# Kernel tuning notes

Measured on AMD Instinct MI355X. Metric: run time of the kernel, lower is better.

## Reference

```python
import jax, jax.numpy as jnp
import numpy as np

B, S, C, HD = 2, 4096, 2048, 128
H = C // HD  # 16 heads
EPS = 1.1920929e-07  # torch RMSNorm default eps for float32 (finfo.eps)


def _make_rope(seq_len, head_dim):
    # Standard RoPE 2x2 rotation matrices: [1, S, 1, head_dim//2, 2, 2]
    half = head_dim // 2
    freqs = 1.0 / (10000.0 ** (np.arange(0, half, dtype=np.float32) / half))
    ang = np.arange(seq_len, dtype=np.float32)[:, None] * freqs[None, :]  # [S, half]
    cos, sin = np.cos(ang), np.sin(ang)
    rot = np.stack([np.stack([cos, -sin], axis=-1),
                    np.stack([sin, cos], axis=-1)], axis=-2)  # [S, half, 2, 2]
    return jnp.asarray(rot[None, :, None])  # [1, S, 1, half, 2, 2]


def setup_inputs() -> dict:
    key = jax.random.key(0)
    ks = jax.random.split(key, 9)
    sc = 1.0 / np.sqrt(C)
    return {
        "x": jax.random.normal(ks[0], (B, S, C), jnp.float32),
        "rope": _make_rope(S, HD),
        "wq": jax.random.normal(ks[1], (C, C), jnp.float32) * sc,
        "bq": jax.random.normal(ks[2], (C,), jnp.float32) * 0.01,
        "wk": jax.random.normal(ks[3], (C, C), jnp.float32) * sc,
        "bk": jax.random.normal(ks[4], (C,), jnp.float32) * 0.01,
        "wv": jax.random.normal(ks[5], (C, C), jnp.float32) * sc,
        "bv": jax.random.normal(ks[6], (C,), jnp.float32) * 0.01,
        "q_norm_w": jnp.ones((HD,), jnp.float32),
        "k_norm_w": jnp.ones((HD,), jnp.float32),
    }


def _rmsnorm(t, w):
    t32 = t.astype(jnp.float32)
    inv = jax.lax.rsqrt(jnp.mean(t32 * t32, axis=-1, keepdims=True) + EPS)
    return (t32 * inv * w).astype(t.dtype)


def _apply_rotary(t, rope):
    # t: [B, S, H, HD] -> pairs [B, S, H, HD//2, 1, 2]; rope: [1, S, 1, HD//2, 2, 2]
    t32 = t.reshape(*t.shape[:-1], HD // 2, 1, 2).astype(jnp.float32)
    out = (rope * t32).sum(axis=-1)  # [B, S, H, HD//2, 2]
    return out.reshape(t.shape).astype(t.dtype)


def reference(x, rope, wq, bq, wk, bk, wv, bv, q_norm_w, k_norm_w):
    # QKV projections (torch Linear: x @ W^T + b)
    q = (jnp.einsum('bsc,oc->bso', x, wq) + bq).reshape(B, S, H, HD)
    k = (jnp.einsum('bsc,oc->bso', x, wk) + bk).reshape(B, S, H, HD)
    v = (jnp.einsum('bsc,oc->bso', x, wv) + bv).reshape(B, S, H, HD)
    # Per-head RMSNorm on q, k (in float32, cast back), then rotary
    q = _apply_rotary(_rmsnorm(q, q_norm_w), rope)
    k = _apply_rotary(_rmsnorm(k, k_norm_w), rope)
    return (q, k, v)
```

## Files before the change

### kernel.cpp

```cpp
#include <hip/hip_runtime.h>


#define M_DIM 8192
#define N_DIM 6144
#define K_DIM 2048
#define NKT 32
#define EPS_RMS 1.1920929e-07f

typedef __bf16 bf16x8 __attribute__((ext_vector_type(8)));
typedef float f32x4 __attribute__((ext_vector_type(4)));

__device__ __forceinline__ void gload16(const void* g, void* l) {
  __builtin_amdgcn_global_load_lds(
      (const __attribute__((address_space(1))) unsigned int*)g,
      (__attribute__((address_space(3))) unsigned int*)l, 16, 0, 0);
}

__device__ __forceinline__ unsigned short f2bf(float f) {
  union { float f; unsigned u; } x; x.f = f;
  unsigned r = x.u + 0x7FFFu + ((x.u >> 16) & 1u);
  return (unsigned short)(r >> 16);
}

__global__ void __launch_bounds__(256) cvt_kernel(const float* __restrict__ s,
                                                  unsigned short* __restrict__ d, int n4) {
  int i = blockIdx.x * blockDim.x + threadIdx.x;
  const int stride = gridDim.x * blockDim.x;
  for (; i < n4; i += stride) {
    const float4 v = reinterpret_cast<const float4*>(s)[i];
    ushort4 o;
    o.x = f2bf(v.x); o.y = f2bf(v.y); o.z = f2bf(v.z); o.w = f2bf(v.w);
    reinterpret_cast<ushort4*>(d)[i] = o;
  }
}

#define LDS4(ARR, BASE, OFF) (*(const f32x4*)((const char*)(ARR) + (BASE) + (OFF)))

#define MFMA_PH(MH, NH)                                                              \
  {                                                                                  \
    _Pragma("unroll")                                                                \
    for (int mf4 = 0; mf4 < 4; ++mf4) {                                              \
      _Pragma("unroll")                                                              \
      for (int nf2 = 0; nf2 < 2; ++nf2) {                                            \
        f32x4& c = acc[(MH) * 4 + mf4][(NH) * 2 + nf2];                              \
        c = __builtin_amdgcn_mfma_f32_16x16x32_bf16(                                 \
            __builtin_bit_cast(bf16x8, Af[mf4][0]),                                  \
            __builtin_bit_cast(bf16x8, Bf[NH][nf2][0]), c, 0, 0, 0);                 \
        c = __builtin_amdgcn_mfma_f32_16x16x32_bf16(                                 \
            __builtin_bit_cast(bf16x8, Af[mf4][1]),                                  \
            __builtin_bit_cast(bf16x8, Bf[NH][nf2][1]), c, 0, 0, 0);                 \
      }                                                                              \
    }                                                                                \
  }

#define FENCE asm volatile("" ::: "memory")

__global__ void __launch_bounds__(512, 2) gemm_fused(
    const unsigned short* __restrict__ xbf, const unsigned short* __restrict__ wbf,
    const float* __restrict__ rope,
    const float* __restrict__ bq, const float* __restrict__ bk, const float* __restrict__ bv,
    const float* __restrict__ qnw, const float* __restrict__ knw,
    float* __restrict__ dout) {
  const int id = blockIdx.x;
  const int xcd = id & 7;
  const int jb = id >> 3;
  const int bm = (xcd << 2) | (jb & 3);
  const int bn = jb >> 2;
  const int m0 = bm << 8, n0 = bn << 8;
  const int tid = threadIdx.x;
  const int w = tid >> 6, l = tid & 63;
  const int l15 = l & 15, lhi = l >> 4;
  const int wr = w >> 2, wc = w & 3;

  __shared__ __align__(16) unsigned short As[32768];
  __shared__ __align__(16) unsigned short Bs[32768];

  const int srow = tid >> 3;
  const int schunk = (tid & 7) ^ (srow & 7);
  const unsigned short* aSrc = xbf + ((size_t)(m0 + srow) << 11) + (schunk << 3);
  const unsigned short* bSrc = wbf + ((size_t)(n0 + srow) << 11) + (schunk << 3);
  char* aDst = (char*)As + (w << 10);
  char* bDst = (char*)Bs + (w << 10);

#define STA(KT, Q) gload16(aSrc + ((size_t)(Q) << 17) + ((KT) << 6), aDst + ((((KT) & 1) << 15) + ((Q) << 13)))
#define STB(KT, Q) gload16(bSrc + ((size_t)(Q) << 17) + ((KT) << 6), bDst + ((((KT) & 1) << 15) + ((Q) << 13)))

  const int sl0 = ((lhi ^ (l15 & 7)) << 4);
  const int sl1 = (((lhi + 4) ^ (l15 & 7)) << 4);
  unsigned a0 = (wr << 14) + (l15 << 7) + sl0;
  unsigned a1 = (wr << 14) + (l15 << 7) + sl1;
  unsigned b0 = (wc << 13) + (l15 << 7) + sl0;
  unsigned b1 = (wc << 13) + (l15 << 7) + sl1;

  f32x4 acc[8][4];
#pragma unroll
  for (int i = 0; i < 8; ++i)
#pragma unroll
    for (int jj = 0; jj < 4; ++jj) acc[i][jj] = (f32x4){0.f, 0.f, 0.f, 0.f};

  f32x4 Af[4][2];
  f32x4 Bf[2][2][2];

  STA(0, 0); STA(0, 1); STA(0, 2); STA(0, 3);
  STB(0, 0); STB(0, 1); STB(0, 2); STB(0, 3);
  asm volatile("s_waitcnt vmcnt(0)" ::: "memory");
  __builtin_amdgcn_s_barrier();
  FENCE;

  for (int kt = 0; kt < NKT; ++kt) {
    const bool notLast = (kt < NKT - 1);
    if (notLast) {
      STA(kt + 1, 0); STA(kt + 1, 1); STA(kt + 1, 2); STA(kt + 1, 3);
      STB(kt + 1, 0); STB(kt + 1, 1); STB(kt + 1, 2); STB(kt + 1, 3);
    }
    Af[0][0] = LDS4(As, a0, 0);        Af[0][1] = LDS4(As, a1, 0);
    Bf[0][0][0] = LDS4(Bs, b0, 0);     Bf[0][0][1] = LDS4(Bs, b1, 0);
    Bf[0][1][0] = LDS4(Bs, b0, 2048);  Bf[0][1][1] = LDS4(Bs, b1, 2048);
    Af[1][0] = LDS4(As, a0, 2048);     Af[1][1] = LDS4(As, a1, 2048);
    Af[2][0] = LDS4(As, a0, 4096);     Af[2][1] = LDS4(As, a1, 4096);
    Af[3][0] = LDS4(As, a0, 6144);     Af[3][1] = LDS4(As, a1, 6144);
    Bf[1][0][0] = LDS4(Bs, b0, 4096);  Bf[1][0][1] = LDS4(Bs, b1, 4096);
    Bf[1][1][0] = LDS4(Bs, b0, 6144);  Bf[1][1][1] = LDS4(Bs, b1, 6144);
    __builtin_amdgcn_s_setprio(1);
    MFMA_PH(0, 0);
    MFMA_PH(0, 1);
    __builtin_amdgcn_s_setprio(0);
    Af[0][0] = LDS4(As, a0, 8192);  Af[0][1] = LDS4(As, a1, 8192);
    Af[1][0] = LDS4(As, a0, 10240); Af[1][1] = LDS4(As, a1, 10240);
    Af[2][0] = LDS4(As, a0, 12288); Af[2][1] = LDS4(As, a1, 12288);
    Af[3][0] = LDS4(As, a0, 14336); Af[3][1] = LDS4(As, a1, 14336);
    __builtin_amdgcn_s_setprio(1);
    MFMA_PH(1, 0);
    MFMA_PH(1, 1);
    __builtin_amdgcn_s_setprio(0);
    asm volatile("s_waitcnt vmcnt(0)" ::: "memory");
    __builtin_amdgcn_s_barrier();
    FENCE;
    a0 ^= 32768u; a1 ^= 32768u; b0 ^= 32768u; b1 ^= 32768u;
  }

  float* scr = (float*)As;
  const int sec = bn >> 3;
  const int nsec = (n0 & 2047) + (wc << 6);
  const float* bias = sec == 0 ? bq : (sec == 1 ? bk : bv);
  float biasv[4];
#pragma unroll
  for (int nf = 0; nf < 4; ++nf) biasv[nf] = bias[nsec + nf * 16 + l15];
  const size_t outBase = ((size_t)sec << 24);

  if (sec < 2) {
    const float* nwp = sec ? knw : qnw;
    const int colh = (wc & 1) << 6;
    float nwv[4];
#pragma unroll
    for (int nf = 0; nf < 4; ++nf) nwv[nf] = nwp[colh + nf * 16 + l15];
    float ssv[8][4];
#pragma unroll
    for (int mf = 0; mf < 8; ++mf) {
#pragma unroll
      for (int jj = 0; jj < 4; ++jj) {
        float ss = 0.f;
#pragma unroll
        for (int nf = 0; nf < 4; ++nf) {
          const float t = acc[mf][nf][jj] + biasv[nf];
          ss += t * t;
        }
        ss += __shfl_xor(ss, 1);
        ss += __shfl_xor(ss, 2);
        ss += __shfl_xor(ss, 4);
        ss += __shfl_xor(ss, 8);
        ssv[mf][jj] = ss;
      }
    }
    if (l15 == 0) {
#pragma unroll
      for (int mf = 0; mf < 8; ++mf)
#pragma unroll
        for (int jj = 0; jj < 4; ++jj)
          scr[(w << 7) + mf * 16 + (lhi << 2) + jj] = ssv[mf][jj];
    }
    __syncthreads();
#pragma unroll
    for (int mf = 0; mf < 8; ++mf) {
#pragma unroll
      for (int jj = 0; jj < 4; ++jj) {
        const float tot = ssv[mf][jj] + scr[((w ^ 1) << 7) + mf * 16 + (lhi << 2) + jj];
        const float inv = rsqrtf(tot * (1.0f / 128.0f) + EPS_RMS);
        const int m = m0 + (wr << 7) + mf * 16 + (lhi << 2) + jj;
        const float* rp = rope + ((size_t)(m & 4095) << 8);
        float* orow = dout + outBase + ((size_t)m << 11) + nsec + l15;
#pragma unroll
        for (int nf = 0; nf < 4; ++nf) {
          const float tn = (acc[mf][nf][jj] + biasv[nf]) * inv * nwv[nf];
          const float pn = __shfl_xor(tn, 1);
          const int ch = colh + nf * 16 + l15;
          const int jr = ch >> 1;
          const float o = fmaf(rp[jr << 2], tn, rp[(jr << 2) + 1 + (ch & 1)] * pn);
          orow[nf << 4] = o;
        }
      }
    }
  } else {
#pragma unroll
    for (int mf = 0; mf < 8; ++mf)
#pragma unroll
      for (int jj = 0; jj < 4; ++jj) {
        const int m = m0 + (wr << 7) + mf * 16 + (lhi << 2) + jj;
        float* orow = dout + outBase + ((size_t)m << 11) + nsec + l15;
#pragma unroll
        for (int nf = 0; nf < 4; ++nf) orow[nf << 4] = acc[mf][nf][jj] + biasv[nf];
      }
  }
}

extern "C" void kernel_launch(void* const* d_in, const int* in_sizes, int n_in,
                              void* d_out, int out_size, void* d_ws, size_t ws_size,
                              hipStream_t stream) {
  const float* x = (const float*)d_in[0];
  const float* rope = (const float*)d_in[1];
  const float* wq = (const float*)d_in[2];
  const float* bq = (const float*)d_in[3];
  const float* wk = (const float*)d_in[4];
  const float* bk = (const float*)d_in[5];
  const float* wv = (const float*)d_in[6];
  const float* bv = (const float*)d_in[7];
  const float* qnw = (const float*)d_in[8];
  const float* knw = (const float*)d_in[9];

  unsigned short* xbf = (unsigned short*)d_ws;
  unsigned short* wbf = xbf + (size_t)M_DIM * K_DIM;

  cvt_kernel<<<2048, 256, 0, stream>>>(x, xbf, M_DIM * K_DIM / 4);
  cvt_kernel<<<1024, 256, 0, stream>>>(wq, wbf, K_DIM * K_DIM / 4);
  cvt_kernel<<<1024, 256, 0, stream>>>(wk, wbf + (size_t)K_DIM * K_DIM, K_DIM * K_DIM / 4);
  cvt_kernel<<<1024, 256, 0, stream>>>(wv, wbf + (size_t)2 * K_DIM * K_DIM, K_DIM * K_DIM / 4);

  gemm_fused<<<(M_DIM / 256) * (N_DIM / 256), 512, 0, stream>>>(
      xbf, wbf, rope, bq, bk, bv, qnw, knw, (float*)d_out);
}
```

Measured before the change: 269.8 us.

## Switch GEMM to 32x32x16 MFMA with split-phase loads and scheduling hints

Replaces the 16x16x32 bf16 MFMA tiling with 32x32x16 instructions: 4x2 f32x16 accumulators per wave and matching swizzled LDS fragment addressing. The K-loop is split into two halves, each with its own barrier and partial vmcnt waits. A-tile global-to-LDS loads are staggered across the halves, and sched_group_barrier hints interleave ds_reads with MFMAs. The RMSNorm/RoPE epilogue is rewritten for the 32x32 output layout. The aim is fewer LDS fragment reads per MFMA and better overlap of loads with compute, at the cost of an extra barrier per iteration and tighter wait-count correctness.

```diff
diff --git a/kernel.cpp b/kernel.cpp
--- a/kernel.cpp
+++ b/kernel.cpp
@@ -9,6 +9,7 @@
 
 typedef __bf16 bf16x8 __attribute__((ext_vector_type(8)));
 typedef float f32x4 __attribute__((ext_vector_type(4)));
+typedef float f32x16 __attribute__((ext_vector_type(16)));
 
 __device__ __forceinline__ void gload16(const void* g, void* l) {
   __builtin_amdgcn_global_load_lds(
@@ -36,19 +37,21 @@
 
 #define LDS4(ARR, BASE, OFF) (*(const f32x4*)((const char*)(ARR) + (BASE) + (OFF)))
 
-#define MFMA_PH(MH, NH)                                                              \
+#define SGB_DS(N)   __builtin_amdgcn_sched_group_barrier(0x100, (N), 0)
+#define SGB_MFMA(N) __builtin_amdgcn_sched_group_barrier(0x8, (N), 0)
+
+#define MFMA_PH32(MH)                                                                \
   {                                                                                  \
     _Pragma("unroll")                                                                \
-    for (int mf4 = 0; mf4 < 4; ++mf4) {                                              \
+    for (int s = 0; s < 4; ++s) {                                                    \
       _Pragma("unroll")                                                              \
-      for (int nf2 = 0; nf2 < 2; ++nf2) {                                            \
-        f32x4& c = acc[(MH) * 4 + mf4][(NH) * 2 + nf2];                              \
-        c = __builtin_amdgcn_mfma_f32_16x16x32_bf16(                                 \
-            __builtin_bit_cast(bf16x8, Af[mf4][0]),                                  \
-            __builtin_bit_cast(bf16x8, Bf[NH][nf2][0]), c, 0, 0, 0);                 \
-        c = __builtin_amdgcn_mfma_f32_16x16x32_bf16(                                 \
-            __builtin_bit_cast(bf16x8, Af[mf4][1]),                                  \
-            __builtin_bit_cast(bf16x8, Bf[NH][nf2][1]), c, 0, 0, 0);                 \
+      for (int mf = 0; mf < 2; ++mf) {                                               \
+        _Pragma("unroll")                                                            \
+        for (int nf = 0; nf < 2; ++nf) {                                             \
+          acc[(MH) * 2 + mf][nf] = __builtin_amdgcn_mfma_f32_32x32x16_bf16(          \
+              __builtin_bit_cast(bf16x8, Af[mf][s]),                                 \
+              __builtin_bit_cast(bf16x8, Bf[nf][s]), acc[(MH) * 2 + mf][nf], 0, 0, 0);\
+        }                                                                            \
       }                                                                              \
     }                                                                                \
   }
@@ -69,7 +72,7 @@
   const int m0 = bm << 8, n0 = bn << 8;
   const int tid = threadIdx.x;
   const int w = tid >> 6, l = tid & 63;
-  const int l15 = l & 15, lhi = l >> 4;
+  const int l31 = l & 31, hi = l >> 5, l7 = l & 7;
   const int wr = w >> 2, wc = w & 3;
 
   __shared__ __align__(16) unsigned short As[32768];
@@ -85,131 +88,139 @@
 #define STA(KT, Q) gload16(aSrc + ((size_t)(Q) << 17) + ((KT) << 6), aDst + ((((KT) & 1) << 15) + ((Q) << 13)))
 #define STB(KT, Q) gload16(bSrc + ((size_t)(Q) << 17) + ((KT) << 6), bDst + ((((KT) & 1) << 15) + ((Q) << 13)))
 
-  const int sl0 = ((lhi ^ (l15 & 7)) << 4);
-  const int sl1 = (((lhi + 4) ^ (l15 & 7)) << 4);
-  unsigned a0 = (wr << 14) + (l15 << 7) + sl0;
-  unsigned a1 = (wr << 14) + (l15 << 7) + sl1;
-  unsigned b0 = (wc << 13) + (l15 << 7) + sl0;
-  unsigned b1 = (wc << 13) + (l15 << 7) + sl1;
-
-  f32x4 acc[8][4];
-#pragma unroll
-  for (int i = 0; i < 8; ++i)
-#pragma unroll
-    for (int jj = 0; jj < 4; ++jj) acc[i][jj] = (f32x4){0.f, 0.f, 0.f, 0.f};
-
-  f32x4 Af[4][2];
-  f32x4 Bf[2][2][2];
-
-  STA(0, 0); STA(0, 1); STA(0, 2); STA(0, 3);
+  unsigned aS0 = (wr << 14) + (l31 << 7) + ((((0 << 1) | hi) ^ l7) << 4);
+  unsigned aS1 = (wr << 14) + (l31 << 7) + ((((1 << 1) | hi) ^ l7) << 4);
+  unsigned aS2 = (wr << 14) + (l31 << 7) + ((((2 << 1) | hi) ^ l7) << 4);
+  unsigned aS3 = (wr << 14) + (l31 << 7) + ((((3 << 1) | hi) ^ l7) << 4);
+  unsigned bS0 = (wc << 13) + (l31 << 7) + ((((0 << 1) | hi) ^ l7) << 4);
+  unsigned bS1 = (wc << 13) + (l31 << 7) + ((((1 << 1) | hi) ^ l7) << 4);
+  unsigned bS2 = (wc << 13) + (l31 << 7) + ((((2 << 1) | hi) ^ l7) << 4);
+  unsigned bS3 = (wc << 13) + (l31 << 7) + ((((3 << 1) | hi) ^ l7) << 4);
+
+  f32x16 acc[4][2];
+#pragma unroll
+  for (int i = 0; i < 4; ++i)
+#pragma unroll
+    for (int jj = 0; jj < 2; ++jj)
+#pragma unroll
+      for (int r = 0; r < 16; ++r) acc[i][jj][r] = 0.f;
+
+  f32x4 Af[2][4];
+  f32x4 Bf[2][4];
+
+  STA(0, 0); STA(0, 2);
   STB(0, 0); STB(0, 1); STB(0, 2); STB(0, 3);
-  asm volatile("s_waitcnt vmcnt(0)" ::: "memory");
+  STA(0, 1); STA(0, 3);
+  asm volatile("s_waitcnt vmcnt(2)" ::: "memory");
   __builtin_amdgcn_s_barrier();
   FENCE;
 
   for (int kt = 0; kt < NKT; ++kt) {
     const bool notLast = (kt < NKT - 1);
+    Af[0][0] = LDS4(As, aS0, 0); Af[1][0] = LDS4(As, aS0, 4096);
+    Bf[0][0] = LDS4(Bs, bS0, 0); Bf[1][0] = LDS4(Bs, bS0, 4096);
+    Af[0][1] = LDS4(As, aS1, 0); Af[1][1] = LDS4(As, aS1, 4096);
+    Bf[0][1] = LDS4(Bs, bS1, 0); Bf[1][1] = LDS4(Bs, bS1, 4096);
+    Af[0][2] = LDS4(As, aS2, 0); Af[1][2] = LDS4(As, aS2, 4096);
+    Bf[0][2] = LDS4(Bs, bS2, 0); Bf[1][2] = LDS4(Bs, bS2, 4096);
+    Af[0][3] = LDS4(As, aS3, 0); Af[1][3] = LDS4(As, aS3, 4096);
+    Bf[0][3] = LDS4(Bs, bS3, 0); Bf[1][3] = LDS4(Bs, bS3, 4096);
     if (notLast) {
-      STA(kt + 1, 0); STA(kt + 1, 1); STA(kt + 1, 2); STA(kt + 1, 3);
+      STA(kt + 1, 0); STA(kt + 1, 2);
       STB(kt + 1, 0); STB(kt + 1, 1); STB(kt + 1, 2); STB(kt + 1, 3);
     }
-    Af[0][0] = LDS4(As, a0, 0);        Af[0][1] = LDS4(As, a1, 0);
-    Bf[0][0][0] = LDS4(Bs, b0, 0);     Bf[0][0][1] = LDS4(Bs, b1, 0);
-    Bf[0][1][0] = LDS4(Bs, b0, 2048);  Bf[0][1][1] = LDS4(Bs, b1, 2048);
-    Af[1][0] = LDS4(As, a0, 2048);     Af[1][1] = LDS4(As, a1, 2048);
-    Af[2][0] = LDS4(As, a0, 4096);     Af[2][1] = LDS4(As, a1, 4096);
-    Af[3][0] = LDS4(As, a0, 6144);     Af[3][1] = LDS4(As, a1, 6144);
-    Bf[1][0][0] = LDS4(Bs, b0, 4096);  Bf[1][0][1] = LDS4(Bs, b1, 4096);
-    Bf[1][1][0] = LDS4(Bs, b0, 6144);  Bf[1][1][1] = LDS4(Bs, b1, 6144);
     __builtin_amdgcn_s_setprio(1);
-    MFMA_PH(0, 0);
-    MFMA_PH(0, 1);
+    MFMA_PH32(0);
+    SGB_DS(8);  SGB_MFMA(4);
+    SGB_DS(4);  SGB_MFMA(4);
+    SGB_DS(4);  SGB_MFMA(8);
     __builtin_amdgcn_s_setprio(0);
-    Af[0][0] = LDS4(As, a0, 8192);  Af[0][1] = LDS4(As, a1, 8192);
-    Af[1][0] = LDS4(As, a0, 10240); Af[1][1] = LDS4(As, a1, 10240);
-    Af[2][0] = LDS4(As, a0, 12288); Af[2][1] = LDS4(As, a1, 12288);
-    Af[3][0] = LDS4(As, a0, 14336); Af[3][1] = LDS4(As, a1, 14336);
-    __builtin_amdgcn_s_setprio(1);
-    MFMA_PH(1, 0);
-    MFMA_PH(1, 1);
-    __builtin_amdgcn_s_setprio(0);
-    asm volatile("s_waitcnt vmcnt(0)" ::: "memory");
+    if (notLast) { asm volatile("s_waitcnt vmcnt(6)" ::: "memory"); }
+    else         { asm volatile("s_waitcnt vmcnt(0)" ::: "memory"); }
     __builtin_amdgcn_s_barrier();
     FENCE;
-    a0 ^= 32768u; a1 ^= 32768u; b0 ^= 32768u; b1 ^= 32768u;
+    Af[0][0] = LDS4(As, aS0, 8192); Af[1][0] = LDS4(As, aS0, 12288);
+    Af[0][1] = LDS4(As, aS1, 8192); Af[1][1] = LDS4(As, aS1, 12288);
+    Af[0][2] = LDS4(As, aS2, 8192); Af[1][2] = LDS4(As, aS2, 12288);
+    Af[0][3] = LDS4(As, aS3, 8192); Af[1][3] = LDS4(As, aS3, 12288);
+    if (notLast) { STA(kt + 1, 1); STA(kt + 1, 3); }
+    __builtin_amdgcn_s_setprio(1);
+    MFMA_PH32(1);
+    SGB_DS(4);  SGB_MFMA(4);
+    SGB_DS(2);  SGB_MFMA(4);
+    SGB_DS(2);  SGB_MFMA(8);
+    __builtin_amdgcn_s_setprio(0);
+    if (notLast) { asm volatile("s_waitcnt vmcnt(2)" ::: "memory"); }
+    __builtin_amdgcn_s_barrier();
+    FENCE;
+    aS0 ^= 32768u; aS1 ^= 32768u; aS2 ^= 32768u; aS3 ^= 32768u;
+    bS0 ^= 32768u; bS1 ^= 32768u; bS2 ^= 32768u; bS3 ^= 32768u;
   }
 
   float* scr = (float*)As;
   const int sec = bn >> 3;
-  const int nsec = (n0 & 2047) + (wc << 6);
+  const int csBase = (n0 & 2047) + (wc << 6) + l31;
   const float* bias = sec == 0 ? bq : (sec == 1 ? bk : bv);
-  float biasv[4];
-#pragma unroll
-  for (int nf = 0; nf < 4; ++nf) biasv[nf] = bias[nsec + nf * 16 + l15];
+  float biasv[2] = {bias[csBase], bias[csBase + 32]};
   const size_t outBase = ((size_t)sec << 24);
 
   if (sec < 2) {
     const float* nwp = sec ? knw : qnw;
-    const int colh = (wc & 1) << 6;
-    float nwv[4];
-#pragma unroll
-    for (int nf = 0; nf < 4; ++nf) nwv[nf] = nwp[colh + nf * 16 + l15];
-    float ssv[8][4];
-#pragma unroll
-    for (int mf = 0; mf < 8; ++mf) {
-#pragma unroll
-      for (int jj = 0; jj < 4; ++jj) {
-        float ss = 0.f;
-#pragma unroll
-        for (int nf = 0; nf < 4; ++nf) {
-          const float t = acc[mf][nf][jj] + biasv[nf];
-          ss += t * t;
-        }
+    const int chBase = ((wc & 1) << 6) + l31;
+    float nwv[2] = {nwp[chBase], nwp[chBase + 32]};
+#pragma unroll
+    for (int mt = 0; mt < 4; ++mt) {
+#pragma unroll
+      for (int r = 0; r < 16; ++r) {
+        const float t0 = acc[mt][0][r] + biasv[0];
+        const float t1 = acc[mt][1][r] + biasv[1];
+        float ss = t0 * t0 + t1 * t1;
         ss += __shfl_xor(ss, 1);
         ss += __shfl_xor(ss, 2);
         ss += __shfl_xor(ss, 4);
         ss += __shfl_xor(ss, 8);
-        ssv[mf][jj] = ss;
+        ss += __shfl_xor(ss, 16);
+        if (l31 == 0) {
+          const int rowf = (r & 3) + ((r >> 2) << 3) + (hi << 2);
+          scr[(w << 7) + (mt << 5) + rowf] = ss;
+        }
       }
     }
-    if (l15 == 0) {
-#pragma unroll
-      for (int mf = 0; mf < 8; ++mf)
-#pragma unroll
-        for (int jj = 0; jj < 4; ++jj)
-          scr[(w << 7) + mf * 16 + (lhi << 2) + jj] = ssv[mf][jj];
-    }
     __syncthreads();
 #pragma unroll
-    for (int mf = 0; mf < 8; ++mf) {
-#pragma unroll
-      for (int jj = 0; jj < 4; ++jj) {
-        const float tot = ssv[mf][jj] + scr[((w ^ 1) << 7) + mf * 16 + (lhi << 2) + jj];
+    for (int mt = 0; mt < 4; ++mt) {
+#pragma unroll
+      for (int r = 0; r < 16; ++r) {
+        const int rowf = (r & 3) + ((r >> 2) << 3) + (hi << 2);
+        const int rloc = (mt << 5) + rowf;
+        const float tot = scr[(w << 7) + rloc] + scr[((w ^ 1) << 7) + rloc];
         const float inv = rsqrtf(tot * (1.0f / 128.0f) + EPS_RMS);
-        const int m = m0 + (wr << 7) + mf * 16 + (lhi << 2) + jj;
+        const int m = m0 + (wr << 7) + rloc;
         const float* rp = rope + ((size_t)(m & 4095) << 8);
-        float* orow = dout + outBase + ((size_t)m << 11) + nsec + l15;
-#pragma unroll
-        for (int nf = 0; nf < 4; ++nf) {
-          const float tn = (acc[mf][nf][jj] + biasv[nf]) * inv * nwv[nf];
+        float* orow = dout + outBase + ((size_t)m << 11) + csBase;
+#pragma unroll
+        for (int nf = 0; nf < 2; ++nf) {
+          const float tn = (acc[mt][nf][r] + biasv[nf]) * inv * nwv[nf];
           const float pn = __shfl_xor(tn, 1);
-          const int ch = colh + nf * 16 + l15;
+          const int ch = chBase + (nf << 5);
           const int jr = ch >> 1;
           const float o = fmaf(rp[jr << 2], tn, rp[(jr << 2) + 1 + (ch & 1)] * pn);
-          orow[nf << 4] = o;
+          orow[nf << 5] = o;
         }
       }
     }
   } else {
 #pragma unroll
-    for (int mf = 0; mf < 8; ++mf)
-#pragma unroll
-      for (int jj = 0; jj < 4; ++jj) {
-        const int m = m0 + (wr << 7) + mf * 16 + (lhi << 2) + jj;
-        float* orow = dout + outBase + ((size_t)m << 11) + nsec + l15;
-#pragma unroll
-        for (int nf = 0; nf < 4; ++nf) orow[nf << 4] = acc[mf][nf][jj] + biasv[nf];
+    for (int mt = 0; mt < 4; ++mt) {
+#pragma unroll
+      for (int r = 0; r < 16; ++r) {
+        const int rowf = (r & 3) + ((r >> 2) << 3) + (hi << 2);
+        const int m = m0 + (wr << 7) + (mt << 5) + rowf;
+        float* orow = dout + outBase + ((size_t)m << 11) + csBase;
+#pragma unroll
+        for (int nf = 0; nf < 2; ++nf) orow[nf << 5] = acc[mt][nf][r] + biasv[nf];
       }
+    }
   }
 }
 
```

Result: slower. 282.5 us (+4.7%).
